# Kernel optimization log

Hardware: AMD Instinct MI355X
Metric: run time of the kernel (lower is better)

## Reference

```python
import jax, jax.numpy as jnp
import numpy as np

B, S, D, H = 2, 2048, 1024, 16
DK = D // H  # 64

def setup_inputs() -> dict:
    key = jax.random.key(0)
    ks = jax.random.split(key, 12)
    scale = 1.0 / np.sqrt(D)
    return {
        "q": jax.random.normal(ks[0], (B, S, D), jnp.float32),
        "k": jax.random.normal(ks[1], (B, S, D), jnp.float32),
        "v": jax.random.normal(ks[2], (B, S, D), jnp.float32),
        "Wq": jax.random.normal(ks[3], (D, D), jnp.float32) * scale,
        "bq": jnp.zeros((D,), jnp.float32),
        "Wk": jax.random.normal(ks[4], (D, D), jnp.float32) * scale,
        "bk": jnp.zeros((D,), jnp.float32),
        "Wv": jax.random.normal(ks[5], (D, D), jnp.float32) * scale,
        "bv": jnp.zeros((D,), jnp.float32),
        "Wo": jax.random.normal(ks[6], (D, D), jnp.float32) * scale,
        "bo": jnp.zeros((D,), jnp.float32),
        "mask": jnp.ones((B, 1, S, S), jnp.bool_),
    }

def reference(q, k, v, Wq, bq, Wk, bk, Wv, bv, Wo, bo, mask):
    # Linear projections: y = x @ W^T + b (torch nn.Linear convention)
    def proj(x, W, b):
        return x @ W.T + b
    # [B,S,D] -> [B,H,S,DK]
    def split_heads(x):
        return x.reshape(B, S, H, DK).transpose(0, 2, 1, 3)

    query = split_heads(proj(q, Wq, bq))
    key_ = split_heads(proj(k, Wk, bk))
    value = split_heads(proj(v, Wv, bv))

    # NOTE: original uses out-of-place masked_fill whose result is discarded,
    # so mask has no effect on the computation (reproduced faithfully here).
    scores = jnp.einsum('bhqd,bhkd->bhqk', query, key_) / jnp.sqrt(
        jnp.asarray(DK, query.dtype))
    attn = jax.nn.softmax(scores, axis=-1)  # dropout p=0.0: identity
    x = jnp.einsum('bhqk,bhkd->bhqd', attn, value)
    x = x.transpose(0, 2, 1, 3).reshape(B, S, D)
    return proj(x, Wo, bo)
```

## Files before the change

kernel.cpp:

```cpp
#include <hip/hip_runtime.h>
#include <hip/hip_bf16.h>


typedef __attribute__((ext_vector_type(8))) short bf16x8;
typedef __attribute__((ext_vector_type(4))) float f32x4;
typedef unsigned short u16;
typedef unsigned int u32;

#define MFMA16(a, b, c) __builtin_amdgcn_mfma_f32_16x16x32_bf16(a, b, c, 0, 0, 0)
#define EXP2(x) __builtin_amdgcn_exp2f(x)

static __device__ __forceinline__ u16 f2bf(float f) {
    union { __hip_bfloat16 h; u16 u; } v;
    v.h = __float2bfloat16(f);
    return v.u;
}

static __device__ __forceinline__ u16 f2bf_fast(float f) {
    return (u16)((__float_as_uint(f) + 0x8000u) >> 16);
}

static __device__ __forceinline__ void gload16(const u16* g, u16* l) {
    __builtin_amdgcn_global_load_lds(
        (const __attribute__((address_space(1))) void*)g,
        (__attribute__((address_space(3))) void*)l, 16, 0, 0);
}

static __device__ __forceinline__ void cvt16(float4 f0, float4 f1,
                                             float4 f2, float4 f3, u16* o) {
    o[0]=f2bf(f0.x);  o[1]=f2bf(f0.y);  o[2]=f2bf(f0.z);  o[3]=f2bf(f0.w);
    o[4]=f2bf(f1.x);  o[5]=f2bf(f1.y);  o[6]=f2bf(f1.z);  o[7]=f2bf(f1.w);
    o[8]=f2bf(f2.x);  o[9]=f2bf(f2.y);  o[10]=f2bf(f2.z); o[11]=f2bf(f2.w);
    o[12]=f2bf(f3.x); o[13]=f2bf(f3.y); o[14]=f2bf(f3.z); o[15]=f2bf(f3.w);
}

struct CvtArgs16 { const float* in[16]; u16* out[16]; };

__global__ __launch_bounds__(256)
void cvt_multi(CvtArgs16 a)
{
    const int tsel = blockIdx.x >> 9;
    const int i = (((blockIdx.x & 511) * 256) + threadIdx.x) * 8;
    const float* in = a.in[tsel];
    u16* out = a.out[tsel];
    float4 x = *(const float4*)(in + i);
    float4 y = *(const float4*)(in + i + 4);
    u16 o[8];
    o[0]=f2bf(x.x); o[1]=f2bf(x.y); o[2]=f2bf(x.z); o[3]=f2bf(x.w);
    o[4]=f2bf(y.x); o[5]=f2bf(y.y); o[6]=f2bf(y.z); o[7]=f2bf(y.w);
    *(uint4*)(out + i) = *(uint4*)o;
}

struct GemmArgs {
    const float* F[3]; const u16* Wb[3]; const float* bias[3];
    u16* C[3]; float osc[3]; int epi[3];
};

__global__ __launch_bounds__(256)
void gemm_qkv(GemmArgs g)
{
    __shared__ u16 lds_f[2][128 * 40];
    __shared__ u16 lds_g[2][128 * 32];

    const int z = blockIdx.y;
    const float* Fp = g.F[z];
    const u16*  Gp = g.Wb[z];
    const int epi = g.epi[z];

    const int t    = threadIdx.x;
    const int lane = t & 63;
    const int w    = t >> 6;
    const int wm   = w >> 1, wn = w & 1;
    const int ll   = lane & 15;
    const int lg   = lane >> 4;

    const int bx  = blockIdx.x;
    const int swz = (bx & 7) * 32 + (bx >> 3);
    const int tile_m = (epi == 1 ? (swz & 7) : (swz >> 3)) * 128;
    const int tile_n = (epi == 1 ? (swz >> 3) : (swz & 7)) * 128;

    const int rowF = (epi == 1) ? tile_n : tile_m;
    const int rowG = (epi == 1) ? tile_m : tile_n;

    const int c0   = w * 2;
    const int lrow = lane >> 2;
    const int lcol = (lane & 3) * 8;

    const int srow = t >> 1;
    const int scol = (t & 1) * 16;
    const float* Fbase = Fp + (size_t)(rowF + srow) * 1024 + scol;
    const u16*   Gb0   = Gp + (size_t)(rowG + c0 * 16 + lrow) * 1024 + lcol;

    f32x4 acc[4][4] = {};

    {
        #pragma unroll
        for (int j = 0; j < 2; j++)
            gload16(Gb0 + (size_t)j * 16 * 1024, &lds_g[0][(c0 + j) * 512]);

        float4 f0 = *(const float4*)(Fbase);
        float4 f1 = *(const float4*)(Fbase + 4);
        float4 f2 = *(const float4*)(Fbase + 8);
        float4 f3 = *(const float4*)(Fbase + 12);
        u16 tmp[16];
        cvt16(f0, f1, f2, f3, tmp);
        *(uint4*)&lds_f[0][srow * 40 + scol]     = *(uint4*)tmp;
        *(uint4*)&lds_f[0][srow * 40 + scol + 8] = *(uint4*)(tmp + 8);
    }
    __syncthreads();

    int cur = 0;
    for (int kt = 0; kt < 1024; kt += 32) {
        const int nxt = cur ^ 1;
        const bool more = (kt + 32 < 1024);

        float4 f0, f1, f2, f3;
        if (more) {
            const float* Fs = Fbase + kt + 32;
            f0 = *(const float4*)(Fs);
            f1 = *(const float4*)(Fs + 4);
            f2 = *(const float4*)(Fs + 8);
            f3 = *(const float4*)(Fs + 12);
            #pragma unroll
            for (int j = 0; j < 2; j++)
                gload16(Gb0 + (size_t)j * 16 * 1024 + kt + 32,
                        &lds_g[nxt][(c0 + j) * 512]);
        }

        const u16* baseA; const u16* baseB; int strA, strB;
        if (epi == 1) { baseA = lds_g[cur]; strA = 32; baseB = lds_f[cur]; strB = 40; }
        else          { baseA = lds_f[cur]; strA = 40; baseB = lds_g[cur]; strB = 32; }

        bf16x8 af[4], bfr[4];
        #pragma unroll
        for (int i = 0; i < 4; i++)
            af[i] = *(bf16x8*)&baseA[(wm * 64 + i * 16 + ll) * strA + lg * 8];
        #pragma unroll
        for (int j = 0; j < 4; j++)
            bfr[j] = *(bf16x8*)&baseB[(wn * 64 + j * 16 + ll) * strB + lg * 8];
        #pragma unroll
        for (int i = 0; i < 4; i++)
            #pragma unroll
            for (int j = 0; j < 4; j++)
                acc[i][j] = MFMA16(af[i], bfr[j], acc[i][j]);

        if (more) {
            u16 tmp[16];
            cvt16(f0, f1, f2, f3, tmp);
            *(uint4*)&lds_f[nxt][srow * 40 + scol]     = *(uint4*)tmp;
            *(uint4*)&lds_f[nxt][srow * 40 + scol + 8] = *(uint4*)(tmp + 8);
        }

        __syncthreads();
        cur = nxt;
    }

    const float osc = g.osc[z];
    const float* bias = g.bias[z];
    u16* Cp = g.C[z];

    #pragma unroll
    for (int i = 0; i < 4; i++) {
        const int row0 = tile_m + wm * 64 + i * 16 + lg * 4;
        #pragma unroll
        for (int j = 0; j < 4; j++) {
            const int col = tile_n + wn * 64 + j * 16 + ll;
            if (epi == 1) {
                const int b = col >> 11, s = col & 2047;
                #pragma unroll
                for (int r = 0; r < 4; r++)
                    Cp[(size_t)(b * 1024 + row0 + r) * 2048 + s] =
                        f2bf(acc[i][j][r] + bias[row0 + r]);
            } else {
                const float bias_v = bias[col];
                const int h = col >> 6, dk = col & 63;
                const int b = row0 >> 11;
                #pragma unroll
                for (int r = 0; r < 4; r++) {
                    const int s = (row0 + r) & 2047;
                    Cp[((size_t)(b * 16 + h) * 2048 + s) * 64 + dk] =
                        f2bf((acc[i][j][r] + bias_v) * osc);
                }
            }
        }
    }
}

__global__ __launch_bounds__(256)
void gemm_out(const u16* __restrict__ Ap, const u16* __restrict__ Wp,
              const float* __restrict__ bias, float* __restrict__ Cp)
{
    __shared__ u16 lds_a[2][128 * 32];
    __shared__ u16 lds_b[2][64 * 32];

    const int t    = threadIdx.x;
    const int lane = t & 63;
    const int w    = t >> 6;
    const int wm   = w >> 1, wn = w & 1;
    const int ll   = lane & 15;
    const int lg   = lane >> 4;

    const int bx  = blockIdx.x;
    const int swz = (bx & 7) * 64 + (bx >> 3);
    const int tile_m = (swz >> 4) * 128;
    const int tile_n = (swz & 15) * 64;

    const int lrow = lane >> 2;
    const int lcol = (lane & 3) * 8;

    f32x4 acc[4][2] = {};

    #define OSTAGE(buf, kt)                                                    \
    {                                                                          \
        _Pragma("unroll")                                                      \
        for (int j = 0; j < 3; j++) {                                          \
            const int c = w * 3 + j;                                           \
            if (c < 8) {                                                       \
                const int row = tile_m + c * 16 + lrow;                        \
                const int col = (kt) + lcol;                                   \
                const u16* ga = Ap + ((size_t)((row >> 11) * 16 + (col >> 6))  \
                                      * 2048 + (row & 2047)) * 64 + (col & 63);\
                gload16(ga, &lds_a[buf][c * 512]);                             \
            } else {                                                           \
                const int cc = c - 8;                                          \
                gload16(Wp + (size_t)(tile_n + cc * 16 + lrow) * 1024          \
                        + (kt) + lcol, &lds_b[buf][cc * 512]);                 \
            }                                                                  \
        }                                                                      \
    }

    OSTAGE(0, 0);
    __syncthreads();

    int cur = 0;
    for (int kt = 0; kt < 1024; kt += 32) {
        if (kt + 32 < 1024) OSTAGE(cur ^ 1, kt + 32);

        bf16x8 af[4], bfr[2];
        #pragma unroll
        for (int i = 0; i < 4; i++)
            af[i] = *(bf16x8*)&lds_a[cur][(wm * 64 + i * 16 + ll) * 32 + lg * 8];
        #pragma unroll
        for (int j = 0; j < 2; j++)
            bfr[j] = *(bf16x8*)&lds_b[cur][(wn * 32 + j * 16 + ll) * 32 + lg * 8];
        #pragma unroll
        for (int i = 0; i < 4; i++)
            #pragma unroll
            for (int j = 0; j < 2; j++)
                acc[i][j] = MFMA16(af[i], bfr[j], acc[i][j]);

        __syncthreads();
        cur ^= 1;
    }
    #undef OSTAGE

    #pragma unroll
    for (int i = 0; i < 4; i++) {
        const int row0 = tile_m + wm * 64 + i * 16 + lg * 4;
        #pragma unroll
        for (int j = 0; j < 2; j++) {
            const int col = tile_n + wn * 32 + j * 16 + ll;
            const float bias_v = bias[col];
            #pragma unroll
            for (int r = 0; r < 4; r++)
                Cp[(size_t)(row0 + r) * 1024 + col] = acc[i][j][r] + bias_v;
        }
    }
}

__global__ __launch_bounds__(512)
void attn_kernel(const u16* __restrict__ Qh, const u16* __restrict__ Kh,
                 const u16* __restrict__ Vt, u16* __restrict__ Oh)
{
    __shared__ u16 lds_k[2][64 * 64];
    __shared__ u16 lds_v[2][64 * 64];
    __shared__ u16 lds_p[8][16 * 64];

    const int t    = threadIdx.x;
    const int lane = t & 63;
    const int w    = t >> 6;
    const int ll   = lane & 15;
    const int lg   = lane >> 4;
    const int r7   = ll & 7;

    const int bx  = blockIdx.x;
    const int swz = (bx & 7) * 64 + (bx >> 3);
    const int qt = swz & 15;
    const int bh = swz >> 4;
    const int q0 = qt * 128 + w * 16;

    const u16* Qbase = Qh + ((size_t)bh * 2048 + q0 + ll) * 64 + lg * 8;
    const bf16x8 bq0 = *(const bf16x8*)(Qbase);
    const bf16x8 bq1 = *(const bf16x8*)(Qbase + 32);

    bf16x8 bones;
    #pragma unroll
    for (int i = 0; i < 8; i++) bones[i] = (short)0x3F80;

    f32x4 acc[4] = {};
    f32x4 acc_l = {};

    const int srow = lane >> 3;
    const int scol = 8 * ((lane & 7) ^ srow);
    const u16* Kg = Kh + (size_t)bh * 2048 * 64;
    const u16* Vg = Vt + (size_t)bh * 64 * 2048;

    #define ASTAGE(buf, kt)                                                    \
    {                                                                          \
        const int rr = w * 8 + srow;                                           \
        gload16(Kg + (size_t)((kt) + rr) * 64 + scol, &lds_k[buf][w * 512]);   \
        gload16(Vg + (size_t)rr * 2048 + (kt) + scol, &lds_v[buf][w * 512]);   \
    }

    ASTAGE(0, 0);
    __syncthreads();

    u16* lp = lds_p[w];
    int cur = 0;

    for (int kt = 0; kt < 2048; kt += 64) {
        if (kt + 64 < 2048) ASTAGE(cur ^ 1, kt + 64);

        f32x4 s[4];
        __builtin_amdgcn_s_setprio(1);
        #pragma unroll
        for (int ks = 0; ks < 4; ks++) {
            const u16* kp = &lds_k[cur][(ks * 16 + ll) * 64];
            const bf16x8 ak0 = *(const bf16x8*)(kp + ((lg * 8)      ^ (r7 * 8)));
            const bf16x8 ak1 = *(const bf16x8*)(kp + ((lg * 8 + 32) ^ (r7 * 8)));
            f32x4 z = {0.f, 0.f, 0.f, 0.f};
            z = MFMA16(ak0, bq0, z);
            z = MFMA16(ak1, bq1, z);
            s[ks] = z;
        }
        __builtin_amdgcn_s_setprio(0);

        #pragma unroll
        for (int ks = 0; ks < 4; ks++) {
            u16 pk[4];
            #pragma unroll
            for (int r = 0; r < 4; r++) pk[r] = f2bf_fast(EXP2(s[ks][r]));
            *(uint2*)&lp[ll * 64 + ((ks * 16 + lg * 4) ^ (r7 * 8))] = *(uint2*)pk;
        }

        __builtin_amdgcn_s_setprio(1);
        #pragma unroll
        for (int ks2 = 0; ks2 < 2; ks2++) {
            const int so = (ks2 * 32 + lg * 8) ^ (r7 * 8);
            const bf16x8 pa = *(const bf16x8*)&lp[ll * 64 + so];
            #pragma unroll
            for (int dt = 0; dt < 4; dt++) {
                const bf16x8 bv = *(const bf16x8*)&lds_v[cur][(dt * 16 + ll) * 64 + so];
                acc[dt] = MFMA16(pa, bv, acc[dt]);
            }
            acc_l = MFMA16(pa, bones, acc_l);
        }
        __builtin_amdgcn_s_setprio(0);

        __syncthreads();
        cur ^= 1;
    }
    #undef ASTAGE

    #pragma unroll
    for (int r = 0; r < 4; r++) {
        const float lq = 1.f / acc_l[r];
        const int qg = q0 + lg * 4 + r;
        u16* Op = Oh + ((size_t)bh * 2048 + qg) * 64 + ll;
        #pragma unroll
        for (int dt = 0; dt < 4; dt++)
            Op[dt * 16] = f2bf(acc[dt][r] * lq);
    }
}

extern "C" void kernel_launch(void* const* d_in, const int* in_sizes, int n_in,
                              void* d_out, int out_size, void* d_ws, size_t ws_size,
                              hipStream_t stream) {
    const float* q  = (const float*)d_in[0];
    const float* k  = (const float*)d_in[1];
    const float* v  = (const float*)d_in[2];
    const float* Wq = (const float*)d_in[3];
    const float* bq = (const float*)d_in[4];
    const float* Wk = (const float*)d_in[5];
    const float* bk = (const float*)d_in[6];
    const float* Wv = (const float*)d_in[7];
    const float* bv = (const float*)d_in[8];
    const float* Wo = (const float*)d_in[9];
    const float* bo = (const float*)d_in[10];
    float* out = (float*)d_out;

    const size_t M4 = (size_t)4 * 1024 * 1024;
    const size_t M1 = (size_t)1024 * 1024;
    const float qscale = 0.18033688011112042f;
    const dim3 blk(256);

    u16* Qh  = (u16*)d_ws;
    u16* Kh  = Qh + M4;
    u16* Vtb = Kh + M4;
    u16* Oh  = Vtb + M4;
    u16* Wqb = Oh + M4;
    u16* Wkb = Wqb + M1;
    u16* Wvb = Wkb + M1;
    u16* Wob = Wvb + M1;

    CvtArgs16 cv;
    for (int j = 0; j < 16; j++) { cv.in[j] = Wq; cv.out[j] = Wqb; }
    cv.in[0]=Wq; cv.out[0]=Wqb;
    cv.in[1]=Wk; cv.out[1]=Wkb;
    cv.in[2]=Wv; cv.out[2]=Wvb;
    cv.in[3]=Wo; cv.out[3]=Wob;
    cvt_multi<<<4 * 512, blk, 0, stream>>>(cv);

    GemmArgs ga;
    ga.F[0]=q;   ga.F[1]=k;   ga.F[2]=v;
    ga.Wb[0]=Wqb; ga.Wb[1]=Wkb; ga.Wb[2]=Wvb;
    ga.bias[0]=bq; ga.bias[1]=bk; ga.bias[2]=bv;
    ga.C[0]=Qh; ga.C[1]=Kh; ga.C[2]=Vtb;
    ga.osc[0]=qscale; ga.osc[1]=1.0f; ga.osc[2]=1.0f;
    ga.epi[0]=3; ga.epi[1]=3; ga.epi[2]=1;
    gemm_qkv<<<dim3(256, 3), blk, 0, stream>>>(ga);

    attn_kernel<<<512, dim3(512), 0, stream>>>(Qh, Kh, Vtb, Oh);

    gemm_out<<<512, blk, 0, stream>>>(Oh, Wob, bo, out);
}
```

Measured before the change: 124.2 us.

## Prefetch fp32 operand two k-steps ahead with manually unrolled double buffer

Rewrites the projection GEMM main loop as a 2x-unrolled ping-pong over the two LDS buffers, with buffer indices fixed at compile time. The fp32 operand is now loaded from global memory two k-steps ahead into alternating register sets, which gives the global load latency more time to be hidden behind MFMA work. In exchange it holds a second set of float4 registers, which adds register pressure and may lower occupancy.

```diff
diff --git a/kernel.cpp b/kernel.cpp
--- a/kernel.cpp
+++ b/kernel.cpp
@@ -93,67 +93,80 @@
 
     f32x4 acc[4][4] = {};
 
-    {
-        #pragma unroll
-        for (int j = 0; j < 2; j++)
-            gload16(Gb0 + (size_t)j * 16 * 1024, &lds_g[0][(c0 + j) * 512]);
-
-        float4 f0 = *(const float4*)(Fbase);
-        float4 f1 = *(const float4*)(Fbase + 4);
-        float4 f2 = *(const float4*)(Fbase + 8);
-        float4 f3 = *(const float4*)(Fbase + 12);
-        u16 tmp[16];
-        cvt16(f0, f1, f2, f3, tmp);
-        *(uint4*)&lds_f[0][srow * 40 + scol]     = *(uint4*)tmp;
-        *(uint4*)&lds_f[0][srow * 40 + scol + 8] = *(uint4*)(tmp + 8);
-    }
+    const u16* fbaseA; const u16* fbaseB; int strA, strB; int selA;
+    if (epi == 1) { selA = 0; strA = 32; strB = 40; }
+    else          { selA = 1; strA = 40; strB = 32; }
+
+    #define DO_MFMA(buf)                                                       \
+    {                                                                          \
+        const u16* bA = selA ? lds_f[buf] : lds_g[buf];                        \
+        const u16* bB = selA ? lds_g[buf] : lds_f[buf];                        \
+        bf16x8 af[4], bfr[4];                                                  \
+        _Pragma("unroll")                                                      \
+        for (int i = 0; i < 4; i++)                                            \
+            af[i] = *(bf16x8*)&bA[(wm * 64 + i * 16 + ll) * strA + lg * 8];    \
+        _Pragma("unroll")                                                      \
+        for (int j = 0; j < 4; j++)                                            \
+            bfr[j] = *(bf16x8*)&bB[(wn * 64 + j * 16 + ll) * strB + lg * 8];   \
+        _Pragma("unroll")                                                      \
+        for (int i = 0; i < 4; i++)                                            \
+            _Pragma("unroll")                                                  \
+            for (int j = 0; j < 4; j++)                                        \
+                acc[i][j] = MFMA16(af[i], bfr[j], acc[i][j]);                  \
+    }
+
+    #define LOAD_F(dst0, dst1, dst2, dst3, s)                                  \
+    {                                                                          \
+        const float* Fs = Fbase + (s) * 32;                                    \
+        dst0 = *(const float4*)(Fs);                                           \
+        dst1 = *(const float4*)(Fs + 4);                                       \
+        dst2 = *(const float4*)(Fs + 8);                                       \
+        dst3 = *(const float4*)(Fs + 12);                                      \
+    }
+
+    #define WRITE_F(buf, s0, s1, s2, s3)                                       \
+    {                                                                          \
+        u16 tmp[16];                                                           \
+        cvt16(s0, s1, s2, s3, tmp);                                            \
+        *(uint4*)&lds_f[buf][srow * 40 + scol]     = *(uint4*)tmp;             \
+        *(uint4*)&lds_f[buf][srow * 40 + scol + 8] = *(uint4*)(tmp + 8);       \
+    }
+
+    #define LOAD_G(buf, s)                                                     \
+    {                                                                          \
+        _Pragma("unroll")                                                      \
+        for (int j = 0; j < 2; j++)                                            \
+            gload16(Gb0 + (size_t)j * 16 * 1024 + (s) * 32,                    \
+                    &lds_g[buf][(c0 + j) * 512]);                              \
+    }
+
+    float4 a0, a1, a2, a3, b0, b1, b2, b3;
+    LOAD_G(0, 0);
+    LOAD_F(a0, a1, a2, a3, 0);
+    WRITE_F(0, a0, a1, a2, a3);
+    LOAD_F(a0, a1, a2, a3, 1);
     __syncthreads();
 
-    int cur = 0;
-    for (int kt = 0; kt < 1024; kt += 32) {
-        const int nxt = cur ^ 1;
-        const bool more = (kt + 32 < 1024);
-
-        float4 f0, f1, f2, f3;
-        if (more) {
-            const float* Fs = Fbase + kt + 32;
-            f0 = *(const float4*)(Fs);
-            f1 = *(const float4*)(Fs + 4);
-            f2 = *(const float4*)(Fs + 8);
-            f3 = *(const float4*)(Fs + 12);
-            #pragma unroll
-            for (int j = 0; j < 2; j++)
-                gload16(Gb0 + (size_t)j * 16 * 1024 + kt + 32,
-                        &lds_g[nxt][(c0 + j) * 512]);
-        }
-
-        const u16* baseA; const u16* baseB; int strA, strB;
-        if (epi == 1) { baseA = lds_g[cur]; strA = 32; baseB = lds_f[cur]; strB = 40; }
-        else          { baseA = lds_f[cur]; strA = 40; baseB = lds_g[cur]; strB = 32; }
-
-        bf16x8 af[4], bfr[4];
-        #pragma unroll
-        for (int i = 0; i < 4; i++)
-            af[i] = *(bf16x8*)&baseA[(wm * 64 + i * 16 + ll) * strA + lg * 8];
-        #pragma unroll
-        for (int j = 0; j < 4; j++)
-            bfr[j] = *(bf16x8*)&baseB[(wn * 64 + j * 16 + ll) * strB + lg * 8];
-        #pragma unroll
-        for (int i = 0; i < 4; i++)
-            #pragma unroll
-            for (int j = 0; j < 4; j++)
-                acc[i][j] = MFMA16(af[i], bfr[j], acc[i][j]);
-
-        if (more) {
-            u16 tmp[16];
-            cvt16(f0, f1, f2, f3, tmp);
-            *(uint4*)&lds_f[nxt][srow * 40 + scol]     = *(uint4*)tmp;
-            *(uint4*)&lds_f[nxt][srow * 40 + scol + 8] = *(uint4*)(tmp + 8);
-        }
-
+    for (int it = 0; it < 16; ++it) {
+        const int s0 = it * 2;
+        if (s0 + 2 < 32) LOAD_F(b0, b1, b2, b3, s0 + 2);
+        if (s0 + 1 < 32) LOAD_G(1, s0 + 1);
+        DO_MFMA(0);
+        if (s0 + 1 < 32) WRITE_F(1, a0, a1, a2, a3);
         __syncthreads();
-        cur = nxt;
-    }
+
+        const int s1 = s0 + 1;
+        if (s1 + 2 < 32) LOAD_F(a0, a1, a2, a3, s1 + 2);
+        if (s1 + 1 < 32) LOAD_G(0, s1 + 1);
+        if (s1 < 32) DO_MFMA(1);
+        if (s1 + 1 < 32) WRITE_F(0, b0, b1, b2, b3);
+        __syncthreads();
+    }
+
+    #undef DO_MFMA
+    #undef LOAD_F
+    #undef WRITE_F
+    #undef LOAD_G
 
     const float osc = g.osc[z];
     const float* bias = g.bias[z];
```

New measurement: 138.5 us. 1.11x slower.
